# Optimization experiments

Measured on AMD Instinct MI355X. Metric: run time of the kernel, lower is better.

Reference implementation:

```python
import jax, jax.numpy as jnp
import numpy as np

T, L, N, DR = 8, 8, 500, 32
D = 2 * DR          # dr2 = 64
K = 12              # neighbors per region
S = 2               # number_sp attention layers


def setup_inputs() -> dict:
    key = jax.random.key(0)
    ks = jax.random.split(key, 14)
    inp = {}
    inp["all_data_static"] = jax.random.normal(ks[0], (T, L, N, D), jnp.float32)
    inp["thre_nc"] = jax.random.uniform(ks[1], (T, L, N, 1), jnp.float32)
    inp["all_data_dynamic_now"] = jax.random.uniform(ks[2], (L, N, D), jnp.float32)
    inp["neigh_poi"] = jax.random.randint(ks[3], (N, K), 0, N)
    inp["neigh_road"] = jax.random.randint(ks[4], (N, K), 0, N)
    inp["neigh_record"] = jax.random.randint(ks[5], (N, K), 0, N)
    inp["w1"] = jax.random.normal(ks[6], (2 * D, D), jnp.float32) * 0.05
    inp["wq_all"] = jax.random.normal(ks[7], (2, 3, S, D, D), jnp.float32) * 0.05
    inp["wk_all"] = jax.random.normal(ks[8], (2, 3, S, D, D), jnp.float32) * 0.05
    inp["wd_all"] = jax.random.normal(ks[9], (2, 3, S, D, D), jnp.float32) * 0.05
    inp["wmix_all"] = jax.random.normal(ks[10], (2, 3, D), jnp.float32) * 0.1
    inp["conv_w"] = jax.random.normal(ks[11], (4, 2 * D + 1), jnp.float32) * 0.05
    inp["conv_b"] = jnp.zeros((4,), jnp.float32)
    inp["fin_w"] = jax.random.normal(ks[12], (N, N), jnp.float32) * 0.02
    inp["fin_b"] = jnp.ones((N,), jnp.float32)
    return inp


def _attention(data, neigh, wq, wk, wd):
    # data: (T,L,N,D), neigh: (N,K)
    dn = data[:, :, neigh, :]                                   # (T,L,N,K,D) gather
    q = jnp.einsum('tlnd,de->tlne', data, wq)                   # (T,L,N,D)
    k = jnp.einsum('tlnkd,de->tlnke', dn, wk)                   # (T,L,N,K,D)
    a = jax.nn.softmax(jnp.einsum('tlne,tlnke->tlnk', q, k), -1)
    out = q + jnp.einsum('tlnk,tlnke->tlne', a, k)              # residual on q
    return jax.nn.sigmoid(jnp.einsum('tlnd,de->tlne', out, wd))


def _multiattention(data, neighs, wq, wk, wd, wmix):
    outs = []
    for g in range(3):  # poi, road, record
        x = data
        for s in range(wq.shape[1]):
            x = _attention(x, neighs[g], wq[g, s], wk[g, s], wd[g, s])
        outs.append(x)
    return jax.nn.sigmoid(outs[0] * wmix[0] + outs[1] * wmix[1] + outs[2] * wmix[2])


def reference(all_data_static, thre_nc, all_data_dynamic_now,
              neigh_poi, neigh_road, neigh_record,
              w1, wq_all, wk_all, wd_all, wmix_all,
              conv_w, conv_b, fin_w, fin_b):
    # --- Evolution: gated recurrence over time steps 1..T-1 ---
    def evo_step(now, xs):
        st, th = xs  # (L,N,D), (L,N,1)
        new = jax.nn.sigmoid(jnp.concatenate([now, st], -1) @ w1 * th
                             + now * (1.0 - th))
        return new, (new, new - now)
    now_final, (dyn_rest, diffs) = jax.lax.scan(
        evo_step, all_data_dynamic_now, (all_data_static[1:], thre_nc[1:]))
    all_dyn = jnp.concatenate([all_data_dynamic_now[None], dyn_rest], 0)  # (T,L,N,D)

    neighs = (neigh_poi, neigh_road, neigh_record)
    dyn = _multiattention(all_dyn, neighs, wq_all[0], wk_all[0], wd_all[0], wmix_all[0])
    sta = _multiattention(all_data_static, neighs, wq_all[1], wk_all[1], wd_all[1], wmix_all[1])
    x = jnp.concatenate([dyn, sta], -1)                          # (T,L,N,2D)

    # --- ConvLSTM, kernel (1,1), hidden_dim=1 -> pointwise gated recurrence ---
    h0 = jnp.zeros((x.shape[0], x.shape[2], 1), x.dtype)         # (T,N,1)
    def cell(carry, xt):  # xt: (T,N,2D)
        h, c = carry
        gates = jnp.concatenate([xt, h], -1) @ conv_w.T + conv_b  # (T,N,4)
        i = jax.nn.sigmoid(gates[..., 0:1])
        f = jax.nn.sigmoid(gates[..., 1:2])
        o = jax.nn.sigmoid(gates[..., 2:3])
        g = jnp.tanh(gates[..., 3:4])
        c2 = f * c + i * g
        h2 = o * jnp.tanh(c2)
        return (h2, c2), None
    (h_last, _), _ = jax.lax.scan(cell, (h0, h0), jnp.swapaxes(x, 0, 1))

    out = jax.nn.sigmoid(h_last[..., 0] @ fin_w.T + fin_b)       # (T,N)
    return out, now_final, diffs
```

## Files before the change

### kernel.cpp

```cpp
#include <hip/hip_runtime.h>
#include <math.h>

namespace {
constexpr int kT = 8, kL = 8, kN = 500, kD = 64, kK = 12;
constexpr int kLN  = kL * kN;
constexpr int kTLN = kT * kL * kN;
constexpr int kBUF = kTLN * kD;
constexpr int XS = 68;
}

__device__ __forceinline__ float sigf(float v) { return 1.f / (1.f + __expf(-v)); }

__device__ __forceinline__ void stage_x(const float* __restrict__ src, float* lds,
                                        int row0, int M) {
    int r  = threadIdx.x >> 4;
    int c4 = (threadIdx.x & 15) << 2;
#pragma unroll
    for (int i = 0; i < 4; ++i) {
        int rr  = r + 16 * i;
        int row = row0 + rr;
        row = row < M ? row : M - 1;
        float4 v = *reinterpret_cast<const float4*>(src + (size_t)row * 64 + c4);
        *reinterpret_cast<float4*>(lds + rr * XS + c4) = v;
    }
}

template <int K>
__device__ __forceinline__ void stage_w(const float* __restrict__ w, float* lds) {
    const float4* s = reinterpret_cast<const float4*>(w);
    float4* d = reinterpret_cast<float4*>(lds);
#pragma unroll
    for (int i = 0; i < K / 16; ++i)
        d[threadIdx.x + 256 * i] = s[threadIdx.x + 256 * i];
}

__device__ __forceinline__ void gemm_core(const float* ldsx, const float* ldsw,
                                          int rblk, int cblk, float4 acc[4]) {
#pragma unroll 4
    for (int k = 0; k < 64; k += 4) {
        float4 xv[4], wv[4];
#pragma unroll
        for (int i = 0; i < 4; ++i)
            xv[i] = *reinterpret_cast<const float4*>(ldsx + (4 * rblk + i) * XS + k);
#pragma unroll
        for (int d = 0; d < 4; ++d)
            wv[d] = *reinterpret_cast<const float4*>(ldsw + (k + d) * 64 + 4 * cblk);
#pragma unroll
        for (int i = 0; i < 4; ++i) {
            float xs[4] = {xv[i].x, xv[i].y, xv[i].z, xv[i].w};
#pragma unroll
            for (int d = 0; d < 4; ++d) {
                acc[i].x = fmaf(xs[d], wv[d].x, acc[i].x);
                acc[i].y = fmaf(xs[d], wv[d].y, acc[i].y);
                acc[i].z = fmaf(xs[d], wv[d].z, acc[i].z);
                acc[i].w = fmaf(xs[d], wv[d].w, acc[i].w);
            }
        }
    }
}

__device__ __forceinline__ void gemm_core2(const float* ldsx, const float* ldswa,
                                           const float* ldswb, int rblk, int cblk,
                                           float4 acca[4], float4 accb[4]) {
#pragma unroll 4
    for (int k = 0; k < 64; k += 4) {
        float4 xv[4], wa[4], wb[4];
#pragma unroll
        for (int i = 0; i < 4; ++i)
            xv[i] = *reinterpret_cast<const float4*>(ldsx + (4 * rblk + i) * XS + k);
#pragma unroll
        for (int d = 0; d < 4; ++d) {
            wa[d] = *reinterpret_cast<const float4*>(ldswa + (k + d) * 64 + 4 * cblk);
            wb[d] = *reinterpret_cast<const float4*>(ldswb + (k + d) * 64 + 4 * cblk);
        }
#pragma unroll
        for (int i = 0; i < 4; ++i) {
            float xs[4] = {xv[i].x, xv[i].y, xv[i].z, xv[i].w};
#pragma unroll
            for (int d = 0; d < 4; ++d) {
                acca[i].x = fmaf(xs[d], wa[d].x, acca[i].x);
                acca[i].y = fmaf(xs[d], wa[d].y, acca[i].y);
                acca[i].z = fmaf(xs[d], wa[d].z, acca[i].z);
                acca[i].w = fmaf(xs[d], wa[d].w, acca[i].w);
                accb[i].x = fmaf(xs[d], wb[d].x, accb[i].x);
                accb[i].y = fmaf(xs[d], wb[d].y, accb[i].y);
                accb[i].z = fmaf(xs[d], wb[d].z, accb[i].z);
                accb[i].w = fmaf(xs[d], wb[d].w, accb[i].w);
            }
        }
    }
}

__global__ void __launch_bounds__(256) evo_all_kernel(const float* __restrict__ stat,
                                                      const float* __restrict__ thre,
                                                      const float* __restrict__ dyn0,
                                                      float* __restrict__ all_dyn,
                                                      float* __restrict__ diff,
                                                      const float* __restrict__ w1) {
    __shared__ float ldsn[64 * XS];
    __shared__ float ldss[64 * XS];
    __shared__ float ldsw[128 * 64];
    int row0 = blockIdx.x * 64;
    stage_x(dyn0, ldsn, row0, kLN);
    stage_w<128>(w1, ldsw);
    int rblk = threadIdx.x >> 4, cblk = threadIdx.x & 15;
#pragma unroll 1
    for (int t = 1; t < kT; ++t) {
        stage_x(stat + (size_t)t * kLN * kD, ldss, row0, kLN);
        __syncthreads();
        float4 acc[4] = {};
        gemm_core(ldsn, ldsw, rblk, cblk, acc);
        gemm_core(ldss, ldsw + 64 * 64, rblk, cblk, acc);
        float4 nv[4];
#pragma unroll
        for (int i = 0; i < 4; ++i) {
            int row = row0 + 4 * rblk + i;
            int rc  = row < kLN ? row : kLN - 1;
            float tt = thre[t * kLN + rc];
            float4 xn = *reinterpret_cast<const float4*>(ldsn + (4 * rblk + i) * XS + 4 * cblk);
            nv[i].x = sigf(acc[i].x * tt + xn.x * (1.f - tt));
            nv[i].y = sigf(acc[i].y * tt + xn.y * (1.f - tt));
            nv[i].z = sigf(acc[i].z * tt + xn.z * (1.f - tt));
            nv[i].w = sigf(acc[i].w * tt + xn.w * (1.f - tt));
            if (row < kLN) {
                float4 df;
                df.x = nv[i].x - xn.x; df.y = nv[i].y - xn.y;
                df.z = nv[i].z - xn.z; df.w = nv[i].w - xn.w;
                *reinterpret_cast<float4*>(all_dyn + ((size_t)t * kLN + row) * 64 + 4 * cblk) = nv[i];
                *reinterpret_cast<float4*>(diff + ((size_t)(t - 1) * kLN + row) * 64 + 4 * cblk) = df;
            }
        }
        __syncthreads();
#pragma unroll
        for (int i = 0; i < 4; ++i)
            *reinterpret_cast<float4*>(ldsn + (4 * rblk + i) * XS + 4 * cblk) = nv[i];
    }
}

__global__ void __launch_bounds__(256) gemm_qk(const float* __restrict__ Xdyn,
                                               const float* __restrict__ Xstat,
                                               const float* __restrict__ wq_all,
                                               const float* __restrict__ wk_all,
                                               float* __restrict__ b1,
                                               float* __restrict__ b2, int step) {
    __shared__ float ldsx[64 * XS];
    __shared__ float ldswq[64 * 64];
    __shared__ float ldswk[64 * 64];
    int c = blockIdx.y;
    int m = c / 3;
    float* b1c = b1 + (size_t)c * kBUF;
    float* b2c = b2 + (size_t)c * kBUF;
    const float* X = step ? b1c : (m == 0 ? Xdyn : Xstat);
    size_t woff = (size_t)(c * 2 + step) * kD * kD;
    int row0 = blockIdx.x * 64;
    stage_x(X, ldsx, row0, kTLN);
    stage_w<64>(wq_all + woff, ldswq);
    stage_w<64>(wk_all + woff, ldswk);
    __syncthreads();
    int rblk = threadIdx.x >> 4, cblk = threadIdx.x & 15;
    float4 aq[4] = {}, ak[4] = {};
    gemm_core2(ldsx, ldswq, ldswk, rblk, cblk, aq, ak);
#pragma unroll
    for (int i = 0; i < 4; ++i) {
        size_t row = row0 + 4 * rblk + i;
        *reinterpret_cast<float4*>(b1c + row * 64 + 4 * cblk) = aq[i];
        *reinterpret_cast<float4*>(b2c + row * 64 + 4 * cblk) = ak[i];
    }
}

__global__ void __launch_bounds__(256) scorewd_kernel(float* __restrict__ b1,
                                                      const float* __restrict__ b2,
                                                      const int* __restrict__ npoi,
                                                      const int* __restrict__ nroad,
                                                      const int* __restrict__ nrec,
                                                      const float* __restrict__ wd_all,
                                                      int step) {
    __shared__ float ldsx[64 * XS];
    __shared__ float ldsw[64 * 64];
    int p   = blockIdx.y * gridDim.x + blockIdx.x;
    int xcd = p & 7;
    int gid = xcd * 375 + (p >> 3);
    int c    = gid / 500;
    int tile = gid - c * 500;
    int g = c % 3;
    float* b1c = b1 + (size_t)c * kBUF;
    const float* b2c = b2 + (size_t)c * kBUF;
    const int* neigh = (g == 0) ? npoi : (g == 1) ? nroad : nrec;
    stage_w<64>(wd_all + (size_t)(c * 2 + step) * kD * kD, ldsw);

    int lane = threadIdx.x & 63;
    int wv   = threadIdx.x >> 6;
    int sub  = lane >> 4;
    int gq   = lane & 15;
    int row0 = tile * 64;
#pragma unroll 1
    for (int pp = 0; pp < 4; ++pp) {
        int lr  = pp * 16 + wv * 4 + sub;
        int row = row0 + lr;
        int n   = row % kN;
        int slab = row - n;
        float4 q = *(reinterpret_cast<const float4*>(b1c) + (size_t)row * 16 + gq);
        const int4* nbp = reinterpret_cast<const int4*>(neigh + n * kK);
        int4 nb0 = nbp[0], nb1 = nbp[1], nb2 = nbp[2];
        int nb[12] = {nb0.x, nb0.y, nb0.z, nb0.w, nb1.x, nb1.y, nb1.z, nb1.w,
                      nb2.x, nb2.y, nb2.z, nb2.w};
        float4 kv[12];
        float sc[12];
#pragma unroll
        for (int j = 0; j < 12; ++j) {
            kv[j] = *(reinterpret_cast<const float4*>(b2c) + (size_t)(slab + nb[j]) * 16 + gq);
            sc[j] = q.x * kv[j].x + q.y * kv[j].y + q.z * kv[j].z + q.w * kv[j].w;
        }
#pragma unroll
        for (int off = 1; off < 16; off <<= 1) {
#pragma unroll
            for (int j = 0; j < 12; ++j) sc[j] += __shfl_xor(sc[j], off, 16);
        }
        float mx = sc[0];
#pragma unroll
        for (int j = 1; j < 12; ++j) mx = fmaxf(mx, sc[j]);
        float ssum = 0.f;
#pragma unroll
        for (int j = 0; j < 12; ++j) { sc[j] = __expf(sc[j] - mx); ssum += sc[j]; }
        float inv = 1.f / ssum;
        float4 o = q;
#pragma unroll
        for (int j = 0; j < 12; ++j) {
            float a = sc[j] * inv;
            o.x = fmaf(a, kv[j].x, o.x);
            o.y = fmaf(a, kv[j].y, o.y);
            o.z = fmaf(a, kv[j].z, o.z);
            o.w = fmaf(a, kv[j].w, o.w);
        }
        *reinterpret_cast<float4*>(ldsx + lr * XS + 4 * gq) = o;
    }
    __syncthreads();
    int rblk = threadIdx.x >> 4, cblk = threadIdx.x & 15;
    float4 acc[4] = {};
    gemm_core(ldsx, ldsw, rblk, cblk, acc);
#pragma unroll
    for (int i = 0; i < 4; ++i) {
        size_t idx = ((size_t)(row0 + 4 * rblk + i)) * 64 + 4 * cblk;
        float4 y;
        y.x = sigf(acc[i].x); y.y = sigf(acc[i].y);
        y.z = sigf(acc[i].z); y.w = sigf(acc[i].w);
        *reinterpret_cast<float4*>(b1c + idx) = y;
    }
}

__global__ void mix_kernel(const float* __restrict__ b1, const float* __restrict__ wmix,
                           float* __restrict__ mixd, float* __restrict__ mixs) {
    int i = blockIdx.x * 256 + threadIdx.x;
    int d = i & 63;
    float vd = b1[i] * wmix[0 * 64 + d]
             + b1[i + (size_t)kBUF] * wmix[1 * 64 + d]
             + b1[i + 2 * (size_t)kBUF] * wmix[2 * 64 + d];
    float vs = b1[i + 3 * (size_t)kBUF] * wmix[3 * 64 + d]
             + b1[i + 4 * (size_t)kBUF] * wmix[4 * 64 + d]
             + b1[i + 5 * (size_t)kBUF] * wmix[5 * 64 + d];
    mixd[i] = sigf(vd);
    mixs[i] = sigf(vs);
}

__global__ void __launch_bounds__(256) lstm_kernel(const float* __restrict__ md,
                                                   const float* __restrict__ ms,
                                                   const float* __restrict__ cw,
                                                   const float* __restrict__ cb,
                                                   float* __restrict__ hlast) {
    int lane = threadIdx.x & 63;
    int wv   = threadIdx.x >> 6;
    int sub  = lane >> 4;
    int fq   = lane & 15;
    int cell = blockIdx.x * 16 + wv * 4 + sub;
    int t = cell / kN, n = cell % kN;
    float wd_[4][4], ws_[4][4], wh[4], bb[4];
#pragma unroll
    for (int gg = 0; gg < 4; ++gg) {
#pragma unroll
        for (int k = 0; k < 4; ++k) {
            wd_[gg][k] = cw[gg * 129 + fq * 4 + k];
            ws_[gg][k] = cw[gg * 129 + 64 + fq * 4 + k];
        }
        wh[gg] = cw[gg * 129 + 128];
        bb[gg] = cb[gg];
    }
    float h = 0.f, cc = 0.f;
#pragma unroll 1
    for (int l = 0; l < kL; ++l) {
        size_t row = (size_t)(t * kL + l) * kN + n;
        float4 xd = *(reinterpret_cast<const float4*>(md) + row * 16 + fq);
        float4 xs = *(reinterpret_cast<const float4*>(ms) + row * 16 + fq);
        float gsum[4];
#pragma unroll
        for (int gg = 0; gg < 4; ++gg) {
            float v = xd.x * wd_[gg][0] + xd.y * wd_[gg][1]
                    + xd.z * wd_[gg][2] + xd.w * wd_[gg][3];
            v += xs.x * ws_[gg][0] + xs.y * ws_[gg][1]
               + xs.z * ws_[gg][2] + xs.w * ws_[gg][3];
            gsum[gg] = v;
        }
#pragma unroll
        for (int off = 1; off < 16; off <<= 1) {
#pragma unroll
            for (int gg = 0; gg < 4; ++gg) gsum[gg] += __shfl_xor(gsum[gg], off, 16);
        }
        float gi = sigf(gsum[0] + bb[0] + h * wh[0]);
        float gf = sigf(gsum[1] + bb[1] + h * wh[1]);
        float go = sigf(gsum[2] + bb[2] + h * wh[2]);
        float gg_ = tanhf(gsum[3] + bb[3] + h * wh[3]);
        cc = gf * cc + gi * gg_;
        h = go * tanhf(cc);
    }
    if (fq == 0) hlast[cell] = h;
}

__global__ void final_kernel(const float* __restrict__ h, const float* __restrict__ fw,
                             const float* __restrict__ fb, float* __restrict__ out) {
    int wave = threadIdx.x >> 6, lane = threadIdx.x & 63;
    int o = blockIdx.x * 4 + wave;
    int t = o / kN, m = o % kN;
    float acc = 0.f;
    for (int n = lane; n < kN; n += 64)
        acc = fmaf(h[t * kN + n], fw[(size_t)m * kN + n], acc);
#pragma unroll
    for (int off = 32; off > 0; off >>= 1) acc += __shfl_xor(acc, off);
    if (lane == 0) out[o] = sigf(acc + fb[m]);
}

extern "C" void kernel_launch(void* const* d_in, const int* in_sizes, int n_in,
                              void* d_out, int out_size, void* d_ws, size_t ws_size,
                              hipStream_t stream) {
    const float* stat   = (const float*)d_in[0];
    const float* thre   = (const float*)d_in[1];
    const float* dyn0   = (const float*)d_in[2];
    const int*   npoi   = (const int*)d_in[3];
    const int*   nroad  = (const int*)d_in[4];
    const int*   nrec   = (const int*)d_in[5];
    const float* w1     = (const float*)d_in[6];
    const float* wq_all = (const float*)d_in[7];
    const float* wk_all = (const float*)d_in[8];
    const float* wd_all = (const float*)d_in[9];
    const float* wmix   = (const float*)d_in[10];
    const float* conv_w = (const float*)d_in[11];
    const float* conv_b = (const float*)d_in[12];
    const float* fin_w  = (const float*)d_in[13];
    const float* fin_b  = (const float*)d_in[14];

    float* out       = (float*)d_out;
    float* now_final = out + kT * kN;
    float* diffs     = now_final + (size_t)kLN * kD;

    float* ws      = (float*)d_ws;
    float* all_dyn = ws;
    float* b1      = ws + (size_t)kBUF;
    float* b2      = ws + 7 * (size_t)kBUF;
    float* mixd    = ws + 13 * (size_t)kBUF;
    float* mixs    = ws + 14 * (size_t)kBUF;
    float* hlast   = ws + 15 * (size_t)kBUF;

    hipMemcpyAsync(all_dyn, dyn0, sizeof(float) * kLN * kD,
                   hipMemcpyDeviceToDevice, stream);
    evo_all_kernel<<<(kLN + 63) / 64, 256, 0, stream>>>(stat, thre, dyn0,
                                                        all_dyn, diffs, w1);
    hipMemcpyAsync(now_final, all_dyn + (size_t)(kT - 1) * kLN * kD,
                   sizeof(float) * kLN * kD, hipMemcpyDeviceToDevice, stream);

    dim3 agrid(kTLN / 64, 6);
    gemm_qk<<<agrid, 256, 0, stream>>>(all_dyn, stat, wq_all, wk_all, b1, b2, 0);
    scorewd_kernel<<<agrid, 256, 0, stream>>>(b1, b2, npoi, nroad, nrec, wd_all, 0);
    gemm_qk<<<agrid, 256, 0, stream>>>(all_dyn, stat, wq_all, wk_all, b1, b2, 1);
    scorewd_kernel<<<agrid, 256, 0, stream>>>(b1, b2, npoi, nroad, nrec, wd_all, 1);
    mix_kernel<<<kBUF / 256, 256, 0, stream>>>(b1, wmix, mixd, mixs);

    lstm_kernel<<<kT * kN / 16, 256, 0, stream>>>(mixd, mixs, conv_w, conv_b, hlast);
    final_kernel<<<kT * kN / 4, 256, 0, stream>>>(hlast, fin_w, fin_b, out);
}
```

Baseline: 361.6 us.

## Fuse mix into LSTM, drop memcpys, read Wd from global in scorewd

```diff
diff --git a/kernel.cpp b/kernel.cpp
--- a/kernel.cpp
+++ b/kernel.cpp
@@ -45,6 +45,32 @@
 #pragma unroll
         for (int d = 0; d < 4; ++d)
             wv[d] = *reinterpret_cast<const float4*>(ldsw + (k + d) * 64 + 4 * cblk);
+#pragma unroll
+        for (int i = 0; i < 4; ++i) {
+            float xs[4] = {xv[i].x, xv[i].y, xv[i].z, xv[i].w};
+#pragma unroll
+            for (int d = 0; d < 4; ++d) {
+                acc[i].x = fmaf(xs[d], wv[d].x, acc[i].x);
+                acc[i].y = fmaf(xs[d], wv[d].y, acc[i].y);
+                acc[i].z = fmaf(xs[d], wv[d].z, acc[i].z);
+                acc[i].w = fmaf(xs[d], wv[d].w, acc[i].w);
+            }
+        }
+    }
+}
+
+__device__ __forceinline__ void gemm_core_gw(const float* ldsx,
+                                             const float* __restrict__ gw,
+                                             int rblk, int cblk, float4 acc[4]) {
+#pragma unroll 4
+    for (int k = 0; k < 64; k += 4) {
+        float4 xv[4], wv[4];
+#pragma unroll
+        for (int i = 0; i < 4; ++i)
+            xv[i] = *reinterpret_cast<const float4*>(ldsx + (4 * rblk + i) * XS + k);
+#pragma unroll
+        for (int d = 0; d < 4; ++d)
+            wv[d] = *reinterpret_cast<const float4*>(gw + (k + d) * 64 + 4 * cblk);
 #pragma unroll
         for (int i = 0; i < 4; ++i) {
             float xs[4] = {xv[i].x, xv[i].y, xv[i].z, xv[i].w};
@@ -96,6 +122,7 @@
                                                       const float* __restrict__ dyn0,
                                                       float* __restrict__ all_dyn,
                                                       float* __restrict__ diff,
+                                                      float* __restrict__ now_final,
                                                       const float* __restrict__ w1) {
     __shared__ float ldsn[64 * XS];
     __shared__ float ldss[64 * XS];
@@ -104,6 +131,15 @@
     stage_x(dyn0, ldsn, row0, kLN);
     stage_w<128>(w1, ldsw);
     int rblk = threadIdx.x >> 4, cblk = threadIdx.x & 15;
+    __syncthreads();
+#pragma unroll
+    for (int i = 0; i < 4; ++i) {
+        int row = row0 + 4 * rblk + i;
+        if (row < kLN) {
+            float4 x0 = *reinterpret_cast<const float4*>(ldsn + (4 * rblk + i) * XS + 4 * cblk);
+            *reinterpret_cast<float4*>(all_dyn + (size_t)row * 64 + 4 * cblk) = x0;
+        }
+    }
 #pragma unroll 1
     for (int t = 1; t < kT; ++t) {
         stage_x(stat + (size_t)t * kLN * kD, ldss, row0, kLN);
@@ -128,6 +164,8 @@
                 df.z = nv[i].z - xn.z; df.w = nv[i].w - xn.w;
                 *reinterpret_cast<float4*>(all_dyn + ((size_t)t * kLN + row) * 64 + 4 * cblk) = nv[i];
                 *reinterpret_cast<float4*>(diff + ((size_t)(t - 1) * kLN + row) * 64 + 4 * cblk) = df;
+                if (t == kT - 1)
+                    *reinterpret_cast<float4*>(now_final + (size_t)row * 64 + 4 * cblk) = nv[i];
             }
         }
         __syncthreads();
@@ -176,7 +214,6 @@
                                                       const float* __restrict__ wd_all,
                                                       int step) {
     __shared__ float ldsx[64 * XS];
-    __shared__ float ldsw[64 * 64];
     int p   = blockIdx.y * gridDim.x + blockIdx.x;
     int xcd = p & 7;
     int gid = xcd * 375 + (p >> 3);
@@ -186,7 +223,7 @@
     float* b1c = b1 + (size_t)c * kBUF;
     const float* b2c = b2 + (size_t)c * kBUF;
     const int* neigh = (g == 0) ? npoi : (g == 1) ? nroad : nrec;
-    stage_w<64>(wd_all + (size_t)(c * 2 + step) * kD * kD, ldsw);
+    const float* gw = wd_all + (size_t)(c * 2 + step) * kD * kD;
 
     int lane = threadIdx.x & 63;
     int wv   = threadIdx.x >> 6;
@@ -237,7 +274,7 @@
     __syncthreads();
     int rblk = threadIdx.x >> 4, cblk = threadIdx.x & 15;
     float4 acc[4] = {};
-    gemm_core(ldsx, ldsw, rblk, cblk, acc);
+    gemm_core_gw(ldsx, gw, rblk, cblk, acc);
 #pragma unroll
     for (int i = 0; i < 4; ++i) {
         size_t idx = ((size_t)(row0 + 4 * rblk + i)) * 64 + 4 * cblk;
@@ -248,22 +285,8 @@
     }
 }
 
-__global__ void mix_kernel(const float* __restrict__ b1, const float* __restrict__ wmix,
-                           float* __restrict__ mixd, float* __restrict__ mixs) {
-    int i = blockIdx.x * 256 + threadIdx.x;
-    int d = i & 63;
-    float vd = b1[i] * wmix[0 * 64 + d]
-             + b1[i + (size_t)kBUF] * wmix[1 * 64 + d]
-             + b1[i + 2 * (size_t)kBUF] * wmix[2 * 64 + d];
-    float vs = b1[i + 3 * (size_t)kBUF] * wmix[3 * 64 + d]
-             + b1[i + 4 * (size_t)kBUF] * wmix[4 * 64 + d]
-             + b1[i + 5 * (size_t)kBUF] * wmix[5 * 64 + d];
-    mixd[i] = sigf(vd);
-    mixs[i] = sigf(vs);
-}
-
-__global__ void __launch_bounds__(256) lstm_kernel(const float* __restrict__ md,
-                                                   const float* __restrict__ ms,
+__global__ void __launch_bounds__(256) lstm_kernel(const float* __restrict__ b1,
+                                                   const float* __restrict__ wmix,
                                                    const float* __restrict__ cw,
                                                    const float* __restrict__ cb,
                                                    float* __restrict__ hlast) {
@@ -284,12 +307,27 @@
         wh[gg] = cw[gg * 129 + 128];
         bb[gg] = cb[gg];
     }
+    float4 wm[6];
+#pragma unroll
+    for (int j = 0; j < 6; ++j)
+        wm[j] = *reinterpret_cast<const float4*>(wmix + j * 64 + fq * 4);
     float h = 0.f, cc = 0.f;
 #pragma unroll 1
     for (int l = 0; l < kL; ++l) {
-        size_t row = (size_t)(t * kL + l) * kN + n;
-        float4 xd = *(reinterpret_cast<const float4*>(md) + row * 16 + fq);
-        float4 xs = *(reinterpret_cast<const float4*>(ms) + row * 16 + fq);
+        size_t row16 = ((size_t)(t * kL + l) * kN + n) * 16 + fq;
+        float4 y[6];
+#pragma unroll
+        for (int j = 0; j < 6; ++j)
+            y[j] = *(reinterpret_cast<const float4*>(b1) + (size_t)j * (kBUF / 4) + row16);
+        float4 xd, xs;
+        xd.x = sigf(y[0].x * wm[0].x + y[1].x * wm[1].x + y[2].x * wm[2].x);
+        xd.y = sigf(y[0].y * wm[0].y + y[1].y * wm[1].y + y[2].y * wm[2].y);
+        xd.z = sigf(y[0].z * wm[0].z + y[1].z * wm[1].z + y[2].z * wm[2].z);
+        xd.w = sigf(y[0].w * wm[0].w + y[1].w * wm[1].w + y[2].w * wm[2].w);
+        xs.x = sigf(y[3].x * wm[3].x + y[4].x * wm[4].x + y[5].x * wm[5].x);
+        xs.y = sigf(y[3].y * wm[3].y + y[4].y * wm[4].y + y[5].y * wm[5].y);
+        xs.z = sigf(y[3].z * wm[3].z + y[4].z * wm[4].z + y[5].z * wm[5].z);
+        xs.w = sigf(y[3].w * wm[3].w + y[4].w * wm[4].w + y[5].w * wm[5].w);
         float gsum[4];
 #pragma unroll
         for (int gg = 0; gg < 4; ++gg) {
@@ -354,24 +392,17 @@
     float* all_dyn = ws;
     float* b1      = ws + (size_t)kBUF;
     float* b2      = ws + 7 * (size_t)kBUF;
-    float* mixd    = ws + 13 * (size_t)kBUF;
-    float* mixs    = ws + 14 * (size_t)kBUF;
-    float* hlast   = ws + 15 * (size_t)kBUF;
-
-    hipMemcpyAsync(all_dyn, dyn0, sizeof(float) * kLN * kD,
-                   hipMemcpyDeviceToDevice, stream);
+    float* hlast   = ws + 13 * (size_t)kBUF;
+
     evo_all_kernel<<<(kLN + 63) / 64, 256, 0, stream>>>(stat, thre, dyn0,
-                                                        all_dyn, diffs, w1);
-    hipMemcpyAsync(now_final, all_dyn + (size_t)(kT - 1) * kLN * kD,
-                   sizeof(float) * kLN * kD, hipMemcpyDeviceToDevice, stream);
+                                                        all_dyn, diffs, now_final, w1);
 
     dim3 agrid(kTLN / 64, 6);
     gemm_qk<<<agrid, 256, 0, stream>>>(all_dyn, stat, wq_all, wk_all, b1, b2, 0);
     scorewd_kernel<<<agrid, 256, 0, stream>>>(b1, b2, npoi, nroad, nrec, wd_all, 0);
     gemm_qk<<<agrid, 256, 0, stream>>>(all_dyn, stat, wq_all, wk_all, b1, b2, 1);
     scorewd_kernel<<<agrid, 256, 0, stream>>>(b1, b2, npoi, nroad, nrec, wd_all, 1);
-    mix_kernel<<<kBUF / 256, 256, 0, stream>>>(b1, wmix, mixd, mixs);
-
-    lstm_kernel<<<kT * kN / 16, 256, 0, stream>>>(mixd, mixs, conv_w, conv_b, hlast);
+
+    lstm_kernel<<<kT * kN / 16, 256, 0, stream>>>(b1, wmix, conv_w, conv_b, hlast);
     final_kernel<<<kT * kN / 4, 256, 0, stream>>>(hlast, fin_w, fin_b, out);
 }
```

New measurement: 350.7 us. 3.0% less time.
